# Kernel tuning notes

Measured on AMD Instinct MI355X. Metric: run time of the kernel, lower is better.

Reference implementation:

```python
import jax, jax.numpy as jnp
import numpy as np

BN_EPS = 0.001
ALPHA = 10.0
WEIGHT_BIT = 8
ACT_BIT = 8
BIAS_BIT = 16


def _ste_round(x, s):
    # straight-through quantize: round(x*s)/s with identity gradient
    return x + jax.lax.stop_gradient(jnp.round(x * s) / s - x)


def _qsym(x, bit):
    # symmetric per-tensor 'scale' quantization
    s = (2.0 ** (bit - 1) - 1.0) / jnp.maximum(jnp.max(jnp.abs(x)), 1e-8)
    return _ste_round(x, s)


def _qrelu(x, alpha, bit):
    # clipped ReLU to [0, alpha] then uniform quantization to 2^bit - 1 levels
    y = jnp.clip(x, 0.0, alpha)
    s = (2.0 ** bit - 1.0) / alpha
    return _ste_round(y, s)


def _folded_qconv(x, w, b, gamma, beta, mean, var, stride, pad):
    # fold BN into conv weights/bias, then quantize weight (8b) and bias (16b)
    sc = gamma / jnp.sqrt(var + BN_EPS)            # [O]
    wf = _qsym(w * sc[:, None, None, None], WEIGHT_BIT)
    bf = _qsym((b - mean) * sc + beta, BIAS_BIT)
    y = jax.lax.conv_general_dilated(
        x, wf, window_strides=stride, padding=[(pad, pad), (pad, pad)],
        dimension_numbers=('NCHW', 'OIHW', 'NCHW'))
    return y + bf[None, :, None, None]


def setup_inputs() -> dict:
    key = jax.random.key(0)
    ks = jax.random.split(key, 20)
    Cin, Cmid, Cout = 256, 128, 512
    d = {'x': jax.random.normal(ks[0], (32, Cin, 56, 56), dtype=jnp.float32)}

    def mk(k0, o, i, kh, kw, tag):
        kk = jax.random.split(k0, 6)
        fan = i * kh * kw
        d['w' + tag] = jax.random.normal(kk[0], (o, i, kh, kw), jnp.float32) * (fan ** -0.5)
        d['b' + tag] = jax.random.normal(kk[1], (o,), jnp.float32) * 0.01
        d['g' + tag] = 1.0 + jax.random.normal(kk[2], (o,), jnp.float32) * 0.1
        d['be' + tag] = jax.random.normal(kk[3], (o,), jnp.float32) * 0.1
        d['m' + tag] = jax.random.normal(kk[4], (o,), jnp.float32) * 0.1
        d['v' + tag] = jax.random.uniform(kk[5], (o,), jnp.float32) + 0.5

    mk(ks[1], Cmid, Cin, 1, 1, '1')
    mk(ks[2], Cmid, Cmid, 3, 3, '2')
    mk(ks[3], Cout, Cmid, 1, 1, '3')
    return d


def reference(x, w1, b1, g1, be1, m1, v1,
              w2, b2, g2, be2, m2, v2,
              w3, b3, g3, be3, m3, v3):
    out = _folded_qconv(x, w1, b1, g1, be1, m1, v1, (1, 1), 0)
    out = _qrelu(out, ALPHA, ACT_BIT)
    out = _folded_qconv(out, w2, b2, g2, be2, m2, v2, (1, 1), 1)
    out = _qrelu(out, ALPHA, ACT_BIT)
    out = _folded_qconv(out, w3, b3, g3, be3, m3, v3, (1, 1), 0)
    return out
```

## Files before the change

### kernel.cpp

```cpp
#include <hip/hip_runtime.h>
#include <math.h>

typedef int v4i  __attribute__((ext_vector_type(4)));
typedef int v16i __attribute__((ext_vector_type(16)));
typedef short v8s __attribute__((ext_vector_type(8)));
typedef float v16f __attribute__((ext_vector_type(16)));

#define N_IMG 32
#define CIN   256
#define CMID  128
#define COUT  512
#define HWP   3136
#define W58   58
#define PLANE_Q 3456
#define CBSTRIDE (PLANE_Q*16)
#define IMGSTRIDE (8*CBSTRIDE)
#define BSROW 248
#define GUARD 16384
#define BN_EPS_F 1e-3f
#define ALPHA_F  10.0f
#define ARELU_S  25.5f

#define OFF_WQ1   0
#define OFF_WF2   32768
#define OFF_WF3   180224
#define OFF_BQ1   245760
#define OFF_BQ2   245888
#define OFF_BQ3   246016
#define OFF_MAX   246528
#define OFF_Q2    246536
#define OFF_Q3    246664
#define OFF_WQ2I  247296
#define OFF_WQ3I  284160
#define OFF_WBF1  300544
#define ACT1Q_GUARD_B 52582400u
#define ACT1Q_B       (ACT1Q_GUARD_B + GUARD)

__device__ __forceinline__ void async16(const char* g, char* l) {
    __builtin_amdgcn_global_load_lds((const __attribute__((address_space(1))) void*)g,
                                     (__attribute__((address_space(3))) void*)l, 16, 0, 0);
}

__global__ __launch_bounds__(256) void fold_all_kernel(
    const float* __restrict__ w1, const float* __restrict__ g1, const float* __restrict__ v1,
    const float* __restrict__ w2, const float* __restrict__ g2, const float* __restrict__ v2,
    const float* __restrict__ w3, const float* __restrict__ g3, const float* __restrict__ v3,
    const float* __restrict__ b1, const float* __restrict__ be1, const float* __restrict__ m1,
    const float* __restrict__ b2, const float* __restrict__ be2, const float* __restrict__ m2,
    const float* __restrict__ b3, const float* __restrict__ be3, const float* __restrict__ m3,
    float* __restrict__ wq1, float* __restrict__ wf2, float* __restrict__ wf3,
    float* __restrict__ bq1, float* __restrict__ bq2, float* __restrict__ bq3,
    unsigned int* __restrict__ maxw)
{
    __shared__ float red[256];
    const int b = blockIdx.x, t = threadIdx.x;
    if (b < 960) {
        const float *w, *g, *v; float* wf; int inner; unsigned int* mslot; int i;
        if (b < 128)      { w = w1; g = g1; v = v1; wf = wq1; inner = CIN;      mslot = maxw + 0; i = b * 256 + t; }
        else if (b < 704) { w = w2; g = g2; v = v2; wf = wf2; inner = CMID * 9; mslot = maxw + 1; i = (b - 128) * 256 + t; }
        else              { w = w3; g = g3; v = v3; wf = wf3; inner = CMID;     mslot = maxw + 2; i = (b - 704) * 256 + t; }
        int o = i / inner;
        float sc = g[o] / sqrtf(v[o] + BN_EPS_F);
        float val = w[i] * sc;
        wf[i] = val;
        red[t] = fabsf(val);
        __syncthreads();
        for (int s = 128; s > 0; s >>= 1) {
            if (t < s) red[t] = fmaxf(red[t], red[t + s]);
            __syncthreads();
        }
        if (t == 0) atomicMax(mslot, __float_as_uint(red[0]));
    } else {
        const float *bb, *gg, *bebe, *mm, *vv; float* bq; int nn;
        if (b == 960)      { bb = b1; gg = g1; bebe = be1; mm = m1; vv = v1; bq = bq1; nn = CMID; }
        else if (b == 961) { bb = b2; gg = g2; bebe = be2; mm = m2; vv = v2; bq = bq2; nn = CMID; }
        else               { bb = b3; gg = g3; bebe = be3; mm = m3; vv = v3; bq = bq3; nn = COUT; }
        float val0 = 0.f, val1 = 0.f;
        if (t < nn) {
            float sc = gg[t] / sqrtf(vv[t] + BN_EPS_F);
            val0 = (bb[t] - mm[t]) * sc + bebe[t];
        }
        int t2 = t + 256;
        if (t2 < nn) {
            float sc = gg[t2] / sqrtf(vv[t2] + BN_EPS_F);
            val1 = (bb[t2] - mm[t2]) * sc + bebe[t2];
        }
        red[t] = fmaxf(fabsf(val0), fabsf(val1));
        __syncthreads();
        for (int s = 128; s > 0; s >>= 1) {
            if (t < s) red[t] = fmaxf(red[t], red[t + s]);
            __syncthreads();
        }
        float mx = fmaxf(red[0], 1e-8f);
        float s = 32767.0f / mx;
        if (t < nn)  bq[t]  = rintf(val0 * s) / s;
        if (t2 < nn) bq[t2] = rintf(val1 * s) / s;
    }
}

__global__ __launch_bounds__(256) void quant_all_kernel(
    const float* __restrict__ wq1f, const float* __restrict__ wf2, const float* __restrict__ wf3,
    const unsigned int* __restrict__ maxw,
    unsigned short* __restrict__ wbf, char* __restrict__ wq2i, char* __restrict__ wq3i,
    int* __restrict__ Q2, int* __restrict__ Q3)
{
    __shared__ int red[256];
    const int b = blockIdx.x, t = threadIdx.x;
    if (b < 128) {
        int i = b * 256 + t;
        float s = 127.0f / fmaxf(__uint_as_float(maxw[0]), 1e-8f);
        int kb = i >> 10, rem = i & 1023;
        int m = rem >> 3, j = rem & 7;
        int c = kb * 8 + j;
        float k = rintf(wq1f[m * CIN + c] * s);
        wbf[i] = (unsigned short)(__float_as_uint(k) >> 16);
    } else if (b < 256) {
        int m = b - 128;
        float s = 127.0f / fmaxf(__uint_as_float(maxw[1]), 1e-8f);
        int sum = 0;
        for (int idx = t; idx < CMID * 9; idx += 256) {
            int c = idx / 9, tap = idx - c * 9;
            int q = (int)rintf(wf2[(size_t)m * (CMID * 9) + idx] * s);
            wq2i[(size_t)tap * 16384 + (c >> 4) * 2048 + m * 16 + (c & 15)] = (char)q;
            sum += q;
        }
        red[t] = sum;
        __syncthreads();
        for (int st = 128; st > 0; st >>= 1) {
            if (t < st) red[t] += red[t + st];
            __syncthreads();
        }
        if (t == 0) Q2[m] = red[0];
    } else {
        int m = (b - 256) * 2 + (t >> 7), c = t & 127;
        float s = 127.0f / fmaxf(__uint_as_float(maxw[2]), 1e-8f);
        int q = (int)rintf(wf3[(size_t)m * CMID + c] * s);
        wq3i[(size_t)(c >> 4) * 8192 + m * 16 + (c & 15)] = (char)q;
        red[t] = q;
        __syncthreads();
        for (int st = 64; st > 0; st >>= 1) {
            if ((t & 127) < st) red[t] += red[t + st];
            __syncthreads();
        }
        if ((t & 127) == 0) Q3[m] = red[t];
    }
}

__global__ __launch_bounds__(256) void conv1_bf16_kernel(
    const float* __restrict__ X, const unsigned short* __restrict__ Wbf,
    const unsigned int* __restrict__ maxw, const float* __restrict__ bq1,
    char* __restrict__ act1q)
{
    __shared__ char lds[49152];
    char* Bh = lds;
    char* Bm = lds + 16384;
    char* Bl = lds + 32768;
    const int tid = threadIdx.x;
    const int n  = blockIdx.z;
    const int q0 = blockIdx.x * 128;
    const int lane = tid & 63, wid = tid >> 6;
    const int lo = lane & 31, hi = lane >> 5;
    const int wm = wid >> 1, wn = wid & 1;
    const float* Xn = X + (size_t)n * CIN * HWP;

    const int skb = tid >> 5, sqq = tid & 31;
    const int qq0 = q0 + sqq * 4;
    int p_[4];
#pragma unroll
    for (int e = 0; e < 4; e++) {
        int q = qq0 + e;
        int y = q / W58, xx = q - y * W58;
        int p = (y - 1) * 56 + (xx - 1);
        p_[e] = p < 0 ? 0 : (p > HWP - 1 ? HWP - 1 : p);
    }
    const bool fast = (p_[1] == p_[0] + 1) && (p_[2] == p_[0] + 2) && (p_[3] == p_[0] + 3);

    v16f acc[2][2] = {};

    for (int kc = 0; kc < 4; kc++) {
        __syncthreads();
        const float* chbase = Xn + (size_t)(kc * 64 + skb * 8) * HWP;
        float v[8][4];
#pragma unroll
        for (int j = 0; j < 8; j++) {
            const float* cp = chbase + (size_t)j * HWP;
            if (fast) {
                float4 f = *(const float4*)(cp + p_[0]);
                v[j][0] = f.x; v[j][1] = f.y; v[j][2] = f.z; v[j][3] = f.w;
            } else {
#pragma unroll
                for (int e = 0; e < 4; e++) v[j][e] = cp[p_[e]];
            }
        }
#pragma unroll
        for (int e = 0; e < 4; e++) {
            unsigned ph[4], pm_[4], pl[4];
#pragma unroll
            for (int jj = 0; jj < 4; jj++) {
                float a0 = v[2 * jj][e], a1 = v[2 * jj + 1][e];
                unsigned u0 = __float_as_uint(a0), u1 = __float_as_uint(a1);
                unsigned h0 = u0 & 0xFFFF0000u, h1 = u1 & 0xFFFF0000u;
                float r0 = a0 - __uint_as_float(h0), r1 = a1 - __uint_as_float(h1);
                unsigned w0 = __float_as_uint(r0) & 0xFFFF0000u;
                unsigned w1 = __float_as_uint(r1) & 0xFFFF0000u;
                float s0 = r0 - __uint_as_float(w0), s1 = r1 - __uint_as_float(w1);
                unsigned l0 = __float_as_uint(s0) & 0xFFFF0000u;
                unsigned l1 = __float_as_uint(s1) & 0xFFFF0000u;
                ph[jj]  = (h0 >> 16) | h1;
                pm_[jj] = (w0 >> 16) | w1;
                pl[jj]  = (l0 >> 16) | l1;
            }
            int off = (skb * 128 + sqq * 4 + e) * 16;
            *(uint4*)(Bh + off) = make_uint4(ph[0], ph[1], ph[2], ph[3]);
            *(uint4*)(Bm + off) = make_uint4(pm_[0], pm_[1], pm_[2], pm_[3]);
            *(uint4*)(Bl + off) = make_uint4(pl[0], pl[1], pl[2], pl[3]);
        }
        __syncthreads();

        const char* wbase = (const char*)Wbf + kc * 16384;
#pragma unroll
        for (int ks = 0; ks < 4; ks++) {
            v8s a[2];
#pragma unroll
            for (int s = 0; s < 2; s++)
                a[s] = *(const v8s*)(wbase + (((ks * 2 + hi) * 128) + wm * 64 + s * 32 + lo) * 16);
#pragma unroll
            for (int pass = 0; pass < 3; pass++) {
                const char* Bp = (pass == 0) ? Bh : ((pass == 1) ? Bm : Bl);
                v8s b[2];
#pragma unroll
                for (int t = 0; t < 2; t++)
                    b[t] = *(const v8s*)(Bp + ((ks * 2 + hi) * 128 + wn * 64 + t * 32 + lo) * 16);
#pragma unroll
                for (int s = 0; s < 2; s++)
#pragma unroll
                    for (int t = 0; t < 2; t++)
                        acc[s][t] = __builtin_amdgcn_mfma_f32_32x32x16_bf16(a[s], b[t], acc[s][t], 0, 0, 0);
            }
        }
    }

    float inv_s = fmaxf(__uint_as_float(maxw[0]), 1e-8f) / 127.0f;
    __syncthreads();
    char* Cs = lds;
#pragma unroll
    for (int s = 0; s < 2; s++)
#pragma unroll
        for (int t = 0; t < 2; t++) {
            int qloc = wn * 64 + t * 32 + lo;
#pragma unroll
            for (int reg = 0; reg < 16; reg++) {
                int m = wm * 64 + s * 32 + (reg & 3) + 8 * (reg >> 2) + 4 * hi;
                float val = fmaf(acc[s][t][reg], inv_s, bq1[m]);
                val = fminf(fmaxf(val, 0.f), ALPHA_F);
                int k1 = (int)rintf(val * ARELU_S);
                Cs[qloc * 148 + m] = (char)(k1 - 128);
            }
        }
    __syncthreads();
    char* dst = act1q + (size_t)n * IMGSTRIDE + (size_t)q0 * 16;
#pragma unroll
    for (int it = 0; it < 4; it++) {
        int idx = it * 256 + tid;
        int ql = idx >> 3, cb = idx & 7;
        int q = q0 + ql;
        int y = q / W58, xx = q - y * W58;
        int4 w;
        if ((unsigned)(y - 1) < 56u && (unsigned)(xx - 1) < 56u) {
            w.x = *(const int*)(Cs + ql * 148 + cb * 16 + 0);
            w.y = *(const int*)(Cs + ql * 148 + cb * 16 + 4);
            w.z = *(const int*)(Cs + ql * 148 + cb * 16 + 8);
            w.w = *(const int*)(Cs + ql * 148 + cb * 16 + 12);
        } else {
            w = make_int4(0x80808080, 0x80808080, 0x80808080, 0x80808080);
        }
        *(int4*)(dst + (size_t)cb * CBSTRIDE + ql * 16) = w;
    }
}

__global__ __launch_bounds__(256) void conv23_i8_kernel(
    const char* __restrict__ actq, const char* __restrict__ wq2i,
    const char* __restrict__ wq3i,
    const int* __restrict__ Q2, const float* __restrict__ bq2,
    const int* __restrict__ Q3, const float* __restrict__ bq3,
    const unsigned int* __restrict__ maxw, float* __restrict__ out)
{
    __shared__ char lds[48128];
    char* Bs = lds;
    char* Ps = lds + 31744;
    const int tid = threadIdx.x;
    const int n  = blockIdx.z;
    const int q0 = blockIdx.x * 128;
    const int lane = tid & 63, wid = tid >> 6;
    const int lo = lane & 31, hi = lane >> 5;
    const int wm = wid >> 1, wn = wid & 1;

    const char* src = actq + (size_t)n * IMGSTRIDE + (long)(q0 - 59) * 16;
#pragma unroll
    for (int cb = 0; cb < 8; cb++) {
        if (tid < 246)
            async16(src + (size_t)cb * CBSTRIDE + tid * 16, Bs + cb * (BSROW * 16) + tid * 16);
    }
    __syncthreads();

    v16i acc[2][2] = {};
    for (int tap = 0; tap < 9; tap++) {
        const char* wt = wq2i + (size_t)tap * 16384;
        const int tapoff = ((tap / 3) - 1) * W58 + (tap % 3) - 1;
#pragma unroll
        for (int ks = 0; ks < 4; ks++) {
            v4i a[2], b[2];
#pragma unroll
            for (int s = 0; s < 2; s++)
                a[s] = *(const v4i*)(wt + (ks * 2 + hi) * 2048 + (wm * 64 + s * 32 + lo) * 16);
#pragma unroll
            for (int t = 0; t < 2; t++) {
                int ql = 59 + tapoff + wn * 64 + t * 32 + lo;
                b[t] = *(const v4i*)(Bs + ((ks * 2 + hi) * BSROW + ql) * 16);
            }
#pragma unroll
            for (int s = 0; s < 2; s++)
#pragma unroll
                for (int t = 0; t < 2; t++)
                    acc[s][t] = __builtin_amdgcn_mfma_i32_32x32x32_i8(a[s], b[t], acc[s][t], 0, 0, 0);
        }
    }

    float scale2 = fmaxf(__uint_as_float(maxw[1]), 1e-8f) / (127.0f * ARELU_S);
    __syncthreads();
    char* Cs = lds;
#pragma unroll
    for (int s = 0; s < 2; s++)
#pragma unroll
        for (int t = 0; t < 2; t++) {
            int qloc = wn * 64 + t * 32 + lo;
#pragma unroll
            for (int reg = 0; reg < 16; reg++) {
                int m = wm * 64 + s * 32 + (reg & 3) + 8 * (reg >> 2) + 4 * hi;
                float val = fmaf((float)(acc[s][t][reg] + 128 * Q2[m]), scale2, bq2[m]);
                val = fminf(fmaxf(val, 0.f), ALPHA_F);
                int k2 = (int)rintf(val * ARELU_S);
                Cs[qloc * 148 + m] = (char)(k2 - 128);
            }
        }
    __syncthreads();
#pragma unroll
    for (int it = 0; it < 4; it++) {
        int idx = it * 256 + tid;
        int cb = idx >> 7, q = idx & 127;
        int4 w;
        w.x = *(const int*)(Cs + q * 148 + cb * 16 + 0);
        w.y = *(const int*)(Cs + q * 148 + cb * 16 + 4);
        w.z = *(const int*)(Cs + q * 148 + cb * 16 + 8);
        w.w = *(const int*)(Cs + q * 148 + cb * 16 + 12);
        *(int4*)(Ps + cb * 2048 + q * 16) = w;
    }
    __syncthreads();

    float scale3 = fmaxf(__uint_as_float(maxw[2]), 1e-8f) / (127.0f * ARELU_S);
    v4i bf[4][2];
#pragma unroll
    for (int ks = 0; ks < 4; ks++)
#pragma unroll
        for (int t = 0; t < 2; t++)
            bf[ks][t] = *(const v4i*)(Ps + (ks * 2 + hi) * 2048 + (wn * 64 + t * 32 + lo) * 16);

    const int qq = q0 + wn * 64 + lo;
#pragma unroll
    for (int m0i = 0; m0i < 4; m0i++) {
        const int m0 = m0i * 128;
        v16i acc3[2][2] = {};
#pragma unroll
        for (int ks = 0; ks < 4; ks++) {
            v4i a[2];
#pragma unroll
            for (int s = 0; s < 2; s++)
                a[s] = *(const v4i*)(wq3i + (ks * 2 + hi) * 8192 + (m0 + wm * 64 + s * 32 + lo) * 16);
#pragma unroll
            for (int s = 0; s < 2; s++)
#pragma unroll
                for (int t = 0; t < 2; t++)
                    acc3[s][t] = __builtin_amdgcn_mfma_i32_32x32x32_i8(a[s], bf[ks][t], acc3[s][t], 0, 0, 0);
        }
#pragma unroll
        for (int s = 0; s < 2; s++)
#pragma unroll
            for (int t = 0; t < 2; t++) {
                int q = qq + t * 32;
                int y = q / W58, x = q - y * W58;
                if ((unsigned)(y - 1) < 56u && (unsigned)(x - 1) < 56u) {
                    int p = (y - 1) * 56 + (x - 1);
                    float* op = out + (size_t)n * COUT * HWP + p;
#pragma unroll
                    for (int reg = 0; reg < 16; reg++) {
                        int m = m0 + wm * 64 + s * 32 + (reg & 3) + 8 * (reg >> 2) + 4 * hi;
                        op[(size_t)m * HWP] = fmaf((float)(acc3[s][t][reg] + 128 * Q3[m]), scale3, bq3[m]);
                    }
                }
            }
    }
}

extern "C" void kernel_launch(void* const* d_in, const int* in_sizes, int n_in,
                              void* d_out, int out_size, void* d_ws, size_t ws_size,
                              hipStream_t stream) {
    const float* x   = (const float*)d_in[0];
    const float* w1  = (const float*)d_in[1];
    const float* b1  = (const float*)d_in[2];
    const float* g1  = (const float*)d_in[3];
    const float* be1 = (const float*)d_in[4];
    const float* m1  = (const float*)d_in[5];
    const float* v1  = (const float*)d_in[6];
    const float* w2  = (const float*)d_in[7];
    const float* b2  = (const float*)d_in[8];
    const float* g2  = (const float*)d_in[9];
    const float* be2 = (const float*)d_in[10];
    const float* m2  = (const float*)d_in[11];
    const float* v2  = (const float*)d_in[12];
    const float* w3  = (const float*)d_in[13];
    const float* b3  = (const float*)d_in[14];
    const float* g3  = (const float*)d_in[15];
    const float* be3 = (const float*)d_in[16];
    const float* m3  = (const float*)d_in[17];
    const float* v3  = (const float*)d_in[18];

    float* ws  = (float*)d_ws;
    unsigned char* wsb = (unsigned char*)d_ws;
    float* wq1 = ws + OFF_WQ1;
    float* wf2 = ws + OFF_WF2;
    float* wf3 = ws + OFF_WF3;
    float* bq1 = ws + OFF_BQ1;
    float* bq2 = ws + OFF_BQ2;
    float* bq3 = ws + OFF_BQ3;
    unsigned int* maxw = (unsigned int*)(ws + OFF_MAX);
    int* Q2 = (int*)(ws + OFF_Q2);
    int* Q3 = (int*)(ws + OFF_Q3);
    char* wq2i = (char*)(ws + OFF_WQ2I);
    char* wq3i = (char*)(ws + OFF_WQ3I);
    unsigned short* wbf = (unsigned short*)(ws + OFF_WBF1);
    char* act1q = (char*)(wsb + ACT1Q_B);
    float* out  = (float*)d_out;

    hipMemsetAsync(maxw, 0, 12, stream);

    fold_all_kernel<<<963, 256, 0, stream>>>(
        w1, g1, v1, w2, g2, v2, w3, g3, v3,
        b1, be1, m1, b2, be2, m2, b3, be3, m3,
        wq1, wf2, wf3, bq1, bq2, bq3, maxw);

    quant_all_kernel<<<512, 256, 0, stream>>>(wq1, wf2, wf3, maxw, wbf, wq2i, wq3i, Q2, Q3);

    conv1_bf16_kernel<<<dim3(27, 1, 32), 256, 0, stream>>>(x, wbf, maxw, bq1, act1q);
    conv23_i8_kernel<<<dim3(27, 1, 32), 256, 0, stream>>>(act1q, wq2i, wq3i, Q2, bq2, Q3, bq3, maxw, out);
}
```

Baseline: 445.0 us.

## Prefetch next X chunk in conv1 and write packed epilogue directly to MFMA layout

In conv1, the global load of the next 64-channel input chunk is issued before the MFMA loop, so it overlaps with the current chunk's matrix work. Both kernels' epilogues now pack four quantized bytes into one dword and write them straight into the channel-blocked LDS layout. This removes the byte-wise transpose buffer and, in conv23, one barrier and an extra LDS copy pass. Launch bounds now request 3 waves per SIMD, which caps register use and may force spills given the extra prefetch registers.

```diff
diff --git a/kernel.cpp b/kernel.cpp
--- a/kernel.cpp
+++ b/kernel.cpp
@@ -146,7 +146,22 @@
     }
 }
 
-__global__ __launch_bounds__(256) void conv1_bf16_kernel(
+#define LOADX(KC) do {                                                        \
+    const float* chbase = Xn + (size_t)((KC) * 64 + skb * 8) * HWP;           \
+    _Pragma("unroll")                                                         \
+    for (int j = 0; j < 8; j++) {                                             \
+        const float* cp = chbase + (size_t)j * HWP;                           \
+        if (fast) {                                                           \
+            float4 f = *(const float4*)(cp + p_[0]);                          \
+            v[j][0] = f.x; v[j][1] = f.y; v[j][2] = f.z; v[j][3] = f.w;       \
+        } else {                                                              \
+            _Pragma("unroll")                                                 \
+            for (int e = 0; e < 4; e++) v[j][e] = cp[p_[e]];                  \
+        }                                                                     \
+    }                                                                         \
+} while (0)
+
+__global__ __launch_bounds__(256, 3) void conv1_bf16_kernel(
     const float* __restrict__ X, const unsigned short* __restrict__ Wbf,
     const unsigned int* __restrict__ maxw, const float* __restrict__ bq1,
     char* __restrict__ act1q)
@@ -176,22 +191,11 @@
     const bool fast = (p_[1] == p_[0] + 1) && (p_[2] == p_[0] + 2) && (p_[3] == p_[0] + 3);
 
     v16f acc[2][2] = {};
+    float v[8][4];
+    LOADX(0);
 
     for (int kc = 0; kc < 4; kc++) {
         __syncthreads();
-        const float* chbase = Xn + (size_t)(kc * 64 + skb * 8) * HWP;
-        float v[8][4];
-#pragma unroll
-        for (int j = 0; j < 8; j++) {
-            const float* cp = chbase + (size_t)j * HWP;
-            if (fast) {
-                float4 f = *(const float4*)(cp + p_[0]);
-                v[j][0] = f.x; v[j][1] = f.y; v[j][2] = f.z; v[j][3] = f.w;
-            } else {
-#pragma unroll
-                for (int e = 0; e < 4; e++) v[j][e] = cp[p_[e]];
-            }
-        }
 #pragma unroll
         for (int e = 0; e < 4; e++) {
             unsigned ph[4], pm_[4], pl[4];
@@ -215,6 +219,7 @@
             *(uint4*)(Bm + off) = make_uint4(pm_[0], pm_[1], pm_[2], pm_[3]);
             *(uint4*)(Bl + off) = make_uint4(pl[0], pl[1], pl[2], pl[3]);
         }
+        if (kc < 3) LOADX(kc + 1);
         __syncthreads();
 
         const char* wbase = (const char*)Wbf + kc * 16384;
@@ -242,19 +247,25 @@
 
     float inv_s = fmaxf(__uint_as_float(maxw[0]), 1e-8f) / 127.0f;
     __syncthreads();
-    char* Cs = lds;
+    char* Ls = lds;
 #pragma unroll
     for (int s = 0; s < 2; s++)
 #pragma unroll
         for (int t = 0; t < 2; t++) {
             int qloc = wn * 64 + t * 32 + lo;
-#pragma unroll
-            for (int reg = 0; reg < 16; reg++) {
-                int m = wm * 64 + s * 32 + (reg & 3) + 8 * (reg >> 2) + 4 * hi;
-                float val = fmaf(acc[s][t][reg], inv_s, bq1[m]);
-                val = fminf(fmaxf(val, 0.f), ALPHA_F);
-                int k1 = (int)rintf(val * ARELU_S);
-                Cs[qloc * 148 + m] = (char)(k1 - 128);
+            int cb0 = wm * 4 + 2 * s;
+#pragma unroll
+            for (int g = 0; g < 4; g++) {
+                unsigned d = 0;
+#pragma unroll
+                for (int r = 0; r < 4; r++) {
+                    int m = wm * 64 + s * 32 + r + 8 * g + 4 * hi;
+                    float val = fmaf(acc[s][t][g * 4 + r], inv_s, bq1[m]);
+                    val = fminf(fmaxf(val, 0.f), ALPHA_F);
+                    int k1 = (int)rintf(val * ARELU_S);
+                    d |= (unsigned)((k1 - 128) & 255) << (8 * r);
+                }
+                *(unsigned*)(Ls + (cb0 + (g >> 1)) * 2048 + qloc * 16 + (g & 1) * 8 + 4 * hi) = d;
             }
         }
     __syncthreads();
@@ -262,23 +273,19 @@
 #pragma unroll
     for (int it = 0; it < 4; it++) {
         int idx = it * 256 + tid;
-        int ql = idx >> 3, cb = idx & 7;
+        int cb = idx >> 7, ql = idx & 127;
         int q = q0 + ql;
         int y = q / W58, xx = q - y * W58;
         int4 w;
-        if ((unsigned)(y - 1) < 56u && (unsigned)(xx - 1) < 56u) {
-            w.x = *(const int*)(Cs + ql * 148 + cb * 16 + 0);
-            w.y = *(const int*)(Cs + ql * 148 + cb * 16 + 4);
-            w.z = *(const int*)(Cs + ql * 148 + cb * 16 + 8);
-            w.w = *(const int*)(Cs + ql * 148 + cb * 16 + 12);
-        } else {
+        if ((unsigned)(y - 1) < 56u && (unsigned)(xx - 1) < 56u)
+            w = *(const int4*)(Ls + cb * 2048 + ql * 16);
+        else
             w = make_int4(0x80808080, 0x80808080, 0x80808080, 0x80808080);
-        }
         *(int4*)(dst + (size_t)cb * CBSTRIDE + ql * 16) = w;
     }
 }
 
-__global__ __launch_bounds__(256) void conv23_i8_kernel(
+__global__ __launch_bounds__(256, 3) void conv23_i8_kernel(
     const char* __restrict__ actq, const char* __restrict__ wq2i,
     const char* __restrict__ wq3i,
     const int* __restrict__ Q2, const float* __restrict__ bq2,
@@ -327,34 +334,26 @@
     }
 
     float scale2 = fmaxf(__uint_as_float(maxw[1]), 1e-8f) / (127.0f * ARELU_S);
-    __syncthreads();
-    char* Cs = lds;
 #pragma unroll
     for (int s = 0; s < 2; s++)
 #pragma unroll
         for (int t = 0; t < 2; t++) {
             int qloc = wn * 64 + t * 32 + lo;
-#pragma unroll
-            for (int reg = 0; reg < 16; reg++) {
-                int m = wm * 64 + s * 32 + (reg & 3) + 8 * (reg >> 2) + 4 * hi;
-                float val = fmaf((float)(acc[s][t][reg] + 128 * Q2[m]), scale2, bq2[m]);
-                val = fminf(fmaxf(val, 0.f), ALPHA_F);
-                int k2 = (int)rintf(val * ARELU_S);
-                Cs[qloc * 148 + m] = (char)(k2 - 128);
-            }
-        }
-    __syncthreads();
-#pragma unroll
-    for (int it = 0; it < 4; it++) {
-        int idx = it * 256 + tid;
-        int cb = idx >> 7, q = idx & 127;
-        int4 w;
-        w.x = *(const int*)(Cs + q * 148 + cb * 16 + 0);
-        w.y = *(const int*)(Cs + q * 148 + cb * 16 + 4);
-        w.z = *(const int*)(Cs + q * 148 + cb * 16 + 8);
-        w.w = *(const int*)(Cs + q * 148 + cb * 16 + 12);
-        *(int4*)(Ps + cb * 2048 + q * 16) = w;
-    }
+            int cb0 = wm * 4 + 2 * s;
+#pragma unroll
+            for (int g = 0; g < 4; g++) {
+                unsigned d = 0;
+#pragma unroll
+                for (int r = 0; r < 4; r++) {
+                    int m = wm * 64 + s * 32 + r + 8 * g + 4 * hi;
+                    float val = fmaf((float)(acc[s][t][g * 4 + r] + 128 * Q2[m]), scale2, bq2[m]);
+                    val = fminf(fmaxf(val, 0.f), ALPHA_F);
+                    int k2 = (int)rintf(val * ARELU_S);
+                    d |= (unsigned)((k2 - 128) & 255) << (8 * r);
+                }
+                *(unsigned*)(Ps + (cb0 + (g >> 1)) * 2048 + qloc * 16 + (g & 1) * 8 + 4 * hi) = d;
+            }
+        }
     __syncthreads();
 
     float scale3 = fmaxf(__uint_as_float(maxw[2]), 1e-8f) / (127.0f * ARELU_S);
```

After: 458.2 us. +3.0%, slower.
